# Performance work log

Measured on AMD Instinct MI355X. Metric: run time of the kernel, lower is better.

## Reference

```python
import jax, jax.numpy as jnp
import numpy as np

D_MODEL = 1024
N_EXPERTS = 16
TOP_K = 2
D_FF = 512      # per-expert SwiGLU hidden size
D_FF_SHARED = 1024
N_TOKENS = 4096


def setup_inputs() -> dict:
    key = jax.random.key(0)
    ks = jax.random.split(key, 9)
    s_in = 1.0 / np.sqrt(D_MODEL)
    s_ff = 1.0 / np.sqrt(D_FF)
    s_fs = 1.0 / np.sqrt(D_FF_SHARED)
    return {
        "hidden_states": jax.random.normal(ks[0], (N_TOKENS, D_MODEL), jnp.float32),
        "Wg": jax.random.normal(ks[1], (D_MODEL, N_EXPERTS), jnp.float32) * s_in,
        "w1": jax.random.normal(ks[2], (N_EXPERTS, D_MODEL, D_FF), jnp.float32) * s_in,
        "w3": jax.random.normal(ks[3], (N_EXPERTS, D_MODEL, D_FF), jnp.float32) * s_in,
        "w2": jax.random.normal(ks[4], (N_EXPERTS, D_FF, D_MODEL), jnp.float32) * s_ff,
        "ws1": jax.random.normal(ks[5], (D_MODEL, D_FF_SHARED), jnp.float32) * s_in,
        "ws3": jax.random.normal(ks[6], (D_MODEL, D_FF_SHARED), jnp.float32) * s_in,
        "ws2": jax.random.normal(ks[7], (D_FF_SHARED, D_MODEL), jnp.float32) * s_fs,
        "capacity": 1024,
    }


def reference(hidden_states, Wg, w1, w3, w2, ws1, ws3, ws2, capacity):
    T, d = hidden_states.shape
    E = Wg.shape[1]
    C = capacity

    # --- router: softmax in fp32, top-k, renormalize (norm_topk_prob=True) ---
    logits = hidden_states @ Wg                                  # [T, E]
    probs = jax.nn.softmax(logits.astype(jnp.float32), axis=-1)
    topw, topi = jax.lax.top_k(probs, TOP_K)                     # [T, K]
    topw = topw / jnp.sum(topw, axis=-1, keepdims=True)
    topw = topw.astype(hidden_states.dtype)

    # --- dispatch: flatten (token, k) pairs, compute slot within expert buffer ---
    flat_e = topi.reshape(-1)                                    # [T*K] expert id
    flat_t = jnp.repeat(jnp.arange(T), TOP_K)                    # [T*K] source token
    flat_w = topw.reshape(-1)                                    # [T*K]
    oh = jax.nn.one_hot(flat_e, E, dtype=jnp.int32)              # [T*K, E]
    # exclusive position of each pair within its expert's buffer
    pos = jnp.sum((jnp.cumsum(oh, axis=0) - 1) * oh, axis=-1)    # [T*K]
    keep = pos < C
    slot = jnp.where(keep, flat_e * C + pos, E * C)              # dropped -> dummy row

    buf = jnp.zeros((E * C + 1, d), hidden_states.dtype)
    buf = buf.at[slot].set(hidden_states[flat_t])
    xb = buf[: E * C].reshape(E, C, d)                           # [E, C, d]

    # --- per-expert SwiGLU MLP (grouped matmuls) ---
    h = jax.nn.silu(jnp.einsum("ecd,edf->ecf", xb, w1)) * jnp.einsum("ecd,edf->ecf", xb, w3)
    ob = jnp.einsum("ecf,efd->ecd", h, w2).reshape(E * C, d)     # [E*C, d]

    # --- weighted combine: gather expert outputs, scatter-add into token rows ---
    gathered = ob[jnp.minimum(slot, E * C - 1)]                  # [T*K, d]
    y = gathered * (flat_w * keep.astype(flat_w.dtype))[:, None]
    final = jnp.zeros_like(hidden_states).at[flat_t].add(y)

    # --- shared expert (dense SwiGLU over all tokens) ---
    sh = jax.nn.silu(hidden_states @ ws1) * (hidden_states @ ws3)
    final = final + sh @ ws2
    return final
```

## Files before the change

kernel.cpp:

```cpp
#include <hip/hip_runtime.h>
#include <stdint.h>

#define TT 4096
#define DM 1024
#define NE 16
#define DFF 512
#define DFS 1024
#define CAP 1024

typedef unsigned short u16;
typedef __bf16 bf16x8 __attribute__((ext_vector_type(8)));
typedef float f32x4 __attribute__((ext_vector_type(4)));

typedef __attribute__((address_space(1))) void as1_void;
typedef __attribute__((address_space(3))) void as3_void;

__device__ __forceinline__ u16 f2bf(float f) {
  union { float f; uint32_t u; } v; v.f = f;
  uint32_t u = v.u;
  u += 0x7fffu + ((u >> 16) & 1u);
  return (u16)(u >> 16);
}

__device__ __forceinline__ float bf2f(u16 b) {
  union { uint32_t u; float f; } v; v.u = ((uint32_t)b) << 16;
  return v.f;
}

__device__ __forceinline__ void gl2lds16(const void* g, void* l) {
  __builtin_amdgcn_global_load_lds(
      (as1_void*)(uintptr_t)g,
      (as3_void*)(uint32_t)(uintptr_t)l,
      16, 0, 0);
}

__global__ __launch_bounds__(256) void k_prep(
    const float* __restrict__ x, const float* __restrict__ Wg,
    const float* __restrict__ w1, const float* __restrict__ w3,
    const float* __restrict__ w2, const float* __restrict__ ws1,
    const float* __restrict__ ws3, const float* __restrict__ ws2,
    u16* __restrict__ hbf,
    u16* __restrict__ w1t, u16* __restrict__ w3t, u16* __restrict__ w2t,
    u16* __restrict__ ws1t, u16* __restrict__ ws3t, u16* __restrict__ ws2t,
    int* __restrict__ counts, int* __restrict__ tok_slot,
    int* __restrict__ tslot, float* __restrict__ tw) {
  __shared__ __align__(16) char smraw[18496];
  __shared__ int pick_e[32];
  __shared__ int base_sh[16];
  const int bid = blockIdx.x;
  const int tid = threadIdx.x;

  if (bid < 256) {
    float* x_lds = (float*)smraw;
    float (*lg)[17] = (float(*)[17])(smraw + 17408);
    const int e16 = tid & 15;
    const int kpc = tid >> 4;
    const int t0 = bid * 16;
    const int col = (tid & 63) * 4;
    const int rsub = tid >> 6;

    float acc[16];
#pragma unroll
    for (int t = 0; t < 16; ++t) acc[t] = 0.f;

    for (int q = 0; q < 4; ++q) {
      if (q) __syncthreads();
#pragma unroll
      for (int p = 0; p < 4; ++p) {
        int r = p * 4 + rsub;
        float4 xv = *(const float4*)&x[(size_t)(t0 + r) * DM + q * 256 + col];
        ushort4 o;
        o.x = f2bf(xv.x); o.y = f2bf(xv.y); o.z = f2bf(xv.z); o.w = f2bf(xv.w);
        *(ushort4*)&hbf[(size_t)(t0 + r) * DM + q * 256 + col] = o;
        *(float4*)&x_lds[r * 256 + col] = xv;
      }
      __syncthreads();
      float wg[16];
#pragma unroll
      for (int i = 0; i < 16; ++i)
        wg[i] = Wg[(size_t)(q * 256 + kpc * 16 + i) * NE + e16];
#pragma unroll
      for (int t = 0; t < 16; ++t) {
        const float4* xp = (const float4*)&x_lds[t * 256 + kpc * 16];
        float4 a0 = xp[0], a1 = xp[1], a2 = xp[2], a3 = xp[3];
        float s = acc[t];
        s += a0.x * wg[0]  + a0.y * wg[1]  + a0.z * wg[2]  + a0.w * wg[3];
        s += a1.x * wg[4]  + a1.y * wg[5]  + a1.z * wg[6]  + a1.w * wg[7];
        s += a2.x * wg[8]  + a2.y * wg[9]  + a2.z * wg[10] + a2.w * wg[11];
        s += a3.x * wg[12] + a3.y * wg[13] + a3.z * wg[14] + a3.w * wg[15];
        acc[t] = s;
      }
    }
    __syncthreads();
    float* red = (float*)smraw;
#pragma unroll
    for (int t = 0; t < 16; ++t) red[kpc * 272 + t * 16 + e16] = acc[t];
    __syncthreads();
    {
      int t2 = tid >> 4, e2 = tid & 15;
      float s = 0.f;
#pragma unroll
      for (int k2 = 0; k2 < 16; ++k2) s += red[k2 * 272 + t2 * 16 + e2];
      lg[t2][e2] = s;
    }
    __syncthreads();
    if (e16 == 0) {
      int tl = kpc;
      int t = t0 + tl;
      float b0 = -1e30f; int i0 = 0;
#pragma unroll
      for (int i = 0; i < NE; ++i) { float v = lg[tl][i]; if (v > b0) { b0 = v; i0 = i; } }
      float b1 = -1e30f; int i1 = 0;
#pragma unroll
      for (int i = 0; i < NE; ++i) { if (i == i0) continue; float v = lg[tl][i]; if (v > b1) { b1 = v; i1 = i; } }
      float ex = __expf(b1 - b0);
      float w0 = 1.f / (1.f + ex);
      float w1v = 1.f - w0;
      pick_e[2 * tl] = i0;
      pick_e[2 * tl + 1] = i1;
      tw[2 * t] = w0; tw[2 * t + 1] = w1v;
    }
    __syncthreads();
    if (tid < 16) {
      int c = 0;
#pragma unroll
      for (int j = 0; j < 32; ++j) c += (pick_e[j] == tid) ? 1 : 0;
      int base = 0;
      if (c > 0) base = atomicAdd(&counts[tid], c);
      base_sh[tid] = base;
    }
    __syncthreads();
    if (e16 == 0) {
      int tl = kpc;
      int t = t0 + tl;
#pragma unroll
      for (int kk = 0; kk < 2; ++kk) {
        int idx = 2 * tl + kk;
        int e = pick_e[idx];
        int rank = 0;
        for (int j = 0; j < idx; ++j) rank += (pick_e[j] == e) ? 1 : 0;
        int p = base_sh[e] + rank;
        int s = -1;
        if (p < CAP) { s = e * CAP + p; tok_slot[s] = t; }
        tslot[2 * t + kk] = s;
      }
    }
    return;
  }

  int tb = bid - 256;
  int z = tb >> 8, xy = tb & 255;
  const float* ip; u16* op; int R, C;
  if (z < 16)      { ip = w1 + (size_t)z * DM * DFF;       op = w1t + (size_t)z * DM * DFF;       R = DM;  C = DFF; }
  else if (z < 32) { int e = z - 16; ip = w3 + (size_t)e * DM * DFF; op = w3t + (size_t)e * DM * DFF; R = DM;  C = DFF; }
  else if (z < 48) { int e = z - 32; ip = w2 + (size_t)e * DFF * DM; op = w2t + (size_t)e * DFF * DM; R = DFF; C = DM; }
  else if (z == 48){ ip = ws1; op = ws1t; R = DM;  C = DFS; }
  else if (z == 49){ ip = ws3; op = ws3t; R = DM;  C = DFS; }
  else             { ip = ws2; op = ws2t; R = DFS; C = DM; }

  int c0 = (xy & 15) * 64, r0 = (xy >> 4) * 64;
  if (c0 >= C || r0 >= R) return;

  float (*tile)[65] = (float(*)[65])smraw;
  int tx = tid & 15, ty = tid >> 4;
#pragma unroll
  for (int j = 0; j < 4; ++j) {
    int r = ty + 16 * j;
    float4 v = *(const float4*)&ip[(size_t)(r0 + r) * C + c0 + tx * 4];
    *(float4*)&tile[r][tx * 4] = v;
  }
  __syncthreads();
#pragma unroll
  for (int j = 0; j < 4; ++j) {
    int c = ty + 16 * j;
    ushort4 o;
    o.x = f2bf(tile[tx * 4 + 0][c]);
    o.y = f2bf(tile[tx * 4 + 1][c]);
    o.z = f2bf(tile[tx * 4 + 2][c]);
    o.w = f2bf(tile[tx * 4 + 3][c]);
    *(ushort4*)&op[(size_t)(c0 + c) * R + r0 + tx * 4] = o;
  }
}

#define FRAG(BUF, ROW, CC)                                                       \
  (*(const bf16x8*)&BUF[(ROW) * 64 + ((((CC) * 4 + lq) ^ ((ROW) & 7)) << 3)])

__global__ __launch_bounds__(256) void k_up(
    const u16* __restrict__ hbf,
    const u16* __restrict__ ws1t, const u16* __restrict__ ws3t,
    const u16* __restrict__ w1t, const u16* __restrict__ w3t,
    u16* __restrict__ hs, u16* __restrict__ hexp,
    const int* __restrict__ counts, const int* __restrict__ tok_slot) {
  const int tid = threadIdx.x;
  const int nwg = 512 + NE * 64;
  int bid = (int)blockIdx.x;
  bid = (bid & 7) * (nwg >> 3) + (bid >> 3);

  const u16* B1p; const u16* B3p; u16* Cp;
  int m0, n0, N;
  int e = -1, cnt = 0;
  if (bid < 512) {
    m0 = (bid >> 4) * 128; n0 = (bid & 15) * 64;
    B1p = ws1t; B3p = ws3t; Cp = hs; N = DFS;
  } else {
    int r = bid - 512;
    e = r >> 6; int q = r & 63;
    m0 = (q >> 3) * 128; n0 = (q & 7) * 64;
    cnt = counts[e]; if (cnt > CAP) cnt = CAP;
    if (m0 >= cnt) return;
    B1p = w1t + (size_t)e * (DFF * DM);
    B3p = w3t + (size_t)e * (DFF * DM);
    Cp = hexp + (size_t)e * (CAP * DFF);
    N = DFF;
  }

  __shared__ __align__(16) u16 As[2][128 * 64];
  __shared__ __align__(16) u16 Bs1[2][64 * 64];
  __shared__ __align__(16) u16 Bs3[2][64 * 64];

  uint32_t aoff[4], boff[2];
#pragma unroll
  for (int j = 0; j < 4; ++j) {
    int L = tid + 256 * j;
    int row = L >> 3;
    int c = (L & 7) ^ (row & 7);
    int gr;
    if (e >= 0) {
      int rr = m0 + row;
      gr = (rr < cnt) ? tok_slot[e * CAP + rr] : 0;
    } else {
      gr = m0 + row;
    }
    aoff[j] = (uint32_t)gr * DM + c * 8;
  }
#pragma unroll
  for (int j = 0; j < 2; ++j) {
    int L = tid + 256 * j;
    int row = L >> 3;
    int c = (L & 7) ^ (row & 7);
    boff[j] = (uint32_t)(n0 + row) * DM + c * 8;
  }

  const int lane = tid & 63;
  const int wv = tid >> 6;
  const int wr = wv * 32;
  const int lr = lane & 15;
  const int lq = lane >> 4;

  f32x4 acc1[2][4], acc3[2][4];
#pragma unroll
  for (int i = 0; i < 2; ++i)
#pragma unroll
    for (int j = 0; j < 4; ++j) {
      acc1[i][j] = (f32x4){0.f, 0.f, 0.f, 0.f};
      acc3[i][j] = (f32x4){0.f, 0.f, 0.f, 0.f};
    }

#define UP_STAGE(B, K0)                                                              \
  do {                                                                               \
    _Pragma("unroll")                                                                \
    for (int j = 0; j < 4; ++j)                                                      \
      gl2lds16(hbf + aoff[j] + (K0), &As[B][(size_t)(tid + 256 * j) * 8]);           \
    _Pragma("unroll")                                                                \
    for (int j = 0; j < 2; ++j)                                                      \
      gl2lds16(B1p + boff[j] + (K0), &Bs1[B][(size_t)(tid + 256 * j) * 8]);          \
    _Pragma("unroll")                                                                \
    for (int j = 0; j < 2; ++j)                                                      \
      gl2lds16(B3p + boff[j] + (K0), &Bs3[B][(size_t)(tid + 256 * j) * 8]);          \
  } while (0)

#define UP_COMPUTE(B)                                                                \
  do {                                                                               \
    const u16* Ab = &As[B][0];                                                       \
    const u16* B1b = &Bs1[B][0];                                                     \
    const u16* B3b = &Bs3[B][0];                                                     \
    _Pragma("unroll")                                                                \
    for (int cc = 0; cc < 2; ++cc) {                                                 \
      bf16x8 af[2], bf1[4], bf3[4];                                                  \
      _Pragma("unroll")                                                              \
      for (int i = 0; i < 2; ++i) af[i] = FRAG(Ab, wr + i * 16 + lr, cc);            \
      _Pragma("unroll")                                                              \
      for (int j = 0; j < 4; ++j) {                                                  \
        bf1[j] = FRAG(B1b, j * 16 + lr, cc);                                         \
        bf3[j] = FRAG(B3b, j * 16 + lr, cc);                                         \
      }                                                                              \
      _Pragma("unroll")                                                              \
      for (int i = 0; i < 2; ++i)                                                    \
        _Pragma("unroll")                                                            \
        for (int j = 0; j < 4; ++j) {                                                \
          acc1[i][j] = __builtin_amdgcn_mfma_f32_16x16x32_bf16(af[i], bf1[j], acc1[i][j], 0, 0, 0); \
          acc3[i][j] = __builtin_amdgcn_mfma_f32_16x16x32_bf16(af[i], bf3[j], acc3[i][j], 0, 0, 0); \
        }                                                                            \
    }                                                                                \
  } while (0)

  UP_STAGE(0, 0);
  __syncthreads();
  int cur = 0;
  const int NT = DM / 64;
  for (int t = 0; t < NT - 1; ++t) {
    UP_STAGE(cur ^ 1, (t + 1) * 64);
    UP_COMPUTE(cur);
    __syncthreads();
    cur ^= 1;
  }
  UP_COMPUTE(cur);

#pragma unroll
  for (int i = 0; i < 2; ++i)
#pragma unroll
    for (int r = 0; r < 4; ++r) {
      int row = m0 + wr + i * 16 + lq * 4 + r;
      u16* crow = Cp + (size_t)row * N;
#pragma unroll
      for (int j = 0; j < 4; ++j) {
        float v1 = acc1[i][j][r];
        float v3 = acc3[i][j][r];
        float h = (v1 / (1.f + __expf(-v1))) * v3;
        crow[n0 + j * 16 + lr] = f2bf(h);
      }
    }
}

__global__ __launch_bounds__(256) void k_down(
    const u16* __restrict__ hs, const u16* __restrict__ ws2t,
    const u16* __restrict__ hexp, const u16* __restrict__ w2t,
    float* __restrict__ out, u16* __restrict__ ob,
    const int* __restrict__ counts) {
  const int tid = threadIdx.x;
  const int nwg = 512 + NE * 128;
  int bid = (int)blockIdx.x;
  bid = (bid & 7) * (nwg >> 3) + (bid >> 3);

  const u16* Ap; const u16* Bp;
  int m0, n0, K, e = -1;
  if (bid < 512) {
    m0 = (bid >> 4) * 128; n0 = (bid & 15) * 64;
    Ap = hs; Bp = ws2t; K = DFS;
  } else {
    int r = bid - 512;
    e = r >> 7; int q = r & 127;
    m0 = (q >> 4) * 128; n0 = (q & 15) * 64;
    int cnt = counts[e]; if (cnt > CAP) cnt = CAP;
    if (m0 >= cnt) return;
    Ap = hexp + (size_t)e * (CAP * DFF);
    Bp = w2t + (size_t)e * (DM * DFF);
    K = DFF;
  }

  __shared__ __align__(16) u16 As[2][128 * 64];
  __shared__ __align__(16) u16 Bs[2][64 * 64];

  uint32_t aoff[4], boff[2];
#pragma unroll
  for (int j = 0; j < 4; ++j) {
    int L = tid + 256 * j;
    int row = L >> 3;
    int c = (L & 7) ^ (row & 7);
    aoff[j] = (uint32_t)(m0 + row) * K + c * 8;
  }
#pragma unroll
  for (int j = 0; j < 2; ++j) {
    int L = tid + 256 * j;
    int row = L >> 3;
    int c = (L & 7) ^ (row & 7);
    boff[j] = (uint32_t)(n0 + row) * K + c * 8;
  }

  const int lane = tid & 63;
  const int wv = tid >> 6;
  const int wr = wv * 32;
  const int lr = lane & 15;
  const int lq = lane >> 4;

  f32x4 acc[2][4];
#pragma unroll
  for (int i = 0; i < 2; ++i)
#pragma unroll
    for (int j = 0; j < 4; ++j) acc[i][j] = (f32x4){0.f, 0.f, 0.f, 0.f};

#define DN_STAGE(B, K0)                                                              \
  do {                                                                               \
    _Pragma("unroll")                                                                \
    for (int j = 0; j < 4; ++j)                                                      \
      gl2lds16(Ap + aoff[j] + (K0), &As[B][(size_t)(tid + 256 * j) * 8]);            \
    _Pragma("unroll")                                                                \
    for (int j = 0; j < 2; ++j)                                                      \
      gl2lds16(Bp + boff[j] + (K0), &Bs[B][(size_t)(tid + 256 * j) * 8]);            \
  } while (0)

#define DN_COMPUTE(B)                                                                \
  do {                                                                               \
    const u16* Ab = &As[B][0];                                                       \
    const u16* Bb = &Bs[B][0];                                                       \
    _Pragma("unroll")                                                                \
    for (int cc = 0; cc < 2; ++cc) {                                                 \
      bf16x8 af[2], bfr[4];                                                          \
      _Pragma("unroll")                                                              \
      for (int i = 0; i < 2; ++i) af[i] = FRAG(Ab, wr + i * 16 + lr, cc);            \
      _Pragma("unroll")                                                              \
      for (int j = 0; j < 4; ++j) bfr[j] = FRAG(Bb, j * 16 + lr, cc);                \
      _Pragma("unroll")                                                              \
      for (int i = 0; i < 2; ++i)                                                    \
        _Pragma("unroll")                                                            \
        for (int j = 0; j < 4; ++j)                                                  \
          acc[i][j] = __builtin_amdgcn_mfma_f32_16x16x32_bf16(af[i], bfr[j], acc[i][j], 0, 0, 0); \
    }                                                                                \
  } while (0)

  DN_STAGE(0, 0);
  __syncthreads();
  int cur = 0;
  const int NT = K / 64;
  for (int t = 0; t < NT - 1; ++t) {
    DN_STAGE(cur ^ 1, (t + 1) * 64);
    DN_COMPUTE(cur);
    __syncthreads();
    cur ^= 1;
  }
  DN_COMPUTE(cur);

  if (e < 0) {
#pragma unroll
    for (int i = 0; i < 2; ++i)
#pragma unroll
      for (int r = 0; r < 4; ++r) {
        int row = m0 + wr + i * 16 + lq * 4 + r;
        float* orow = out + (size_t)row * DM;
#pragma unroll
        for (int j = 0; j < 4; ++j)
          orow[n0 + j * 16 + lr] = acc[i][j][r];
      }
  } else {
    u16* obase = ob + (size_t)e * CAP * DM;
#pragma unroll
    for (int i = 0; i < 2; ++i)
#pragma unroll
      for (int r = 0; r < 4; ++r) {
        int row = m0 + wr + i * 16 + lq * 4 + r;
        u16* orow = obase + (size_t)row * DM;
#pragma unroll
        for (int j = 0; j < 4; ++j)
          orow[n0 + j * 16 + lr] = f2bf(acc[i][j][r]);
      }
  }
}

__global__ __launch_bounds__(256) void k_combine(
    float* __restrict__ out, const u16* __restrict__ ob,
    const int* __restrict__ tslot, const float* __restrict__ tw) {
  int t = blockIdx.x;
  int c = threadIdx.x * 4;
  int s0 = tslot[2 * t], s1 = tslot[2 * t + 1];
  float w0 = tw[2 * t], w1 = tw[2 * t + 1];
  float4 v = *(float4*)&out[(size_t)t * DM + c];
  if (s0 >= 0) {
    ushort4 o = *(const ushort4*)&ob[(size_t)s0 * DM + c];
    v.x += w0 * bf2f(o.x); v.y += w0 * bf2f(o.y);
    v.z += w0 * bf2f(o.z); v.w += w0 * bf2f(o.w);
  }
  if (s1 >= 0) {
    ushort4 o = *(const ushort4*)&ob[(size_t)s1 * DM + c];
    v.x += w1 * bf2f(o.x); v.y += w1 * bf2f(o.y);
    v.z += w1 * bf2f(o.z); v.w += w1 * bf2f(o.w);
  }
  *(float4*)&out[(size_t)t * DM + c] = v;
}

extern "C" void kernel_launch(void* const* d_in, const int* in_sizes, int n_in,
                              void* d_out, int out_size, void* d_ws, size_t ws_size,
                              hipStream_t stream) {
  (void)in_sizes; (void)n_in; (void)out_size; (void)ws_size;
  const float* x   = (const float*)d_in[0];
  const float* Wg  = (const float*)d_in[1];
  const float* w1  = (const float*)d_in[2];
  const float* w3  = (const float*)d_in[3];
  const float* w2  = (const float*)d_in[4];
  const float* ws1 = (const float*)d_in[5];
  const float* ws3 = (const float*)d_in[6];
  const float* ws2 = (const float*)d_in[7];
  float* out = (float*)d_out;
  char* ws = (char*)d_ws;

  u16* hbf   = (u16*)(ws + 0);
  u16* w1t   = (u16*)(ws + 8388608);
  u16* w3t   = (u16*)(ws + 25165824);
  u16* w2t   = (u16*)(ws + 41943040);
  u16* ws1t  = (u16*)(ws + 58720256);
  u16* ws3t  = (u16*)(ws + 60817408);
  u16* ws2t  = (u16*)(ws + 62914560);
  u16* hs    = (u16*)(ws + 65011712);
  u16* hexp  = (u16*)(ws + 73400320);
  int* counts    = (int*)(ws + 90177536);
  int* tok_slot  = (int*)(ws + 90177792);
  int* tslot     = (int*)(ws + 90243328);
  float* tw      = (float*)(ws + 90276096);
  u16* ob    = (u16*)(ws + 0);

  hipMemsetAsync(counts, 0, NE * sizeof(int), stream);

  k_prep<<<dim3(256 + 51 * 256), dim3(256), 0, stream>>>(
      x, Wg, w1, w3, w2, ws1, ws3, ws2,
      hbf, w1t, w3t, w2t, ws1t, ws3t, ws2t,
      counts, tok_slot, tslot, tw);

  k_up<<<dim3(512 + NE * 64), dim3(256), 0, stream>>>(
      hbf, ws1t, ws3t, w1t, w3t, hs, hexp, counts, tok_slot);

  k_down<<<dim3(512 + NE * 128), dim3(256), 0, stream>>>(
      hs, ws2t, hexp, w2t, out, ob, counts);

  k_combine<<<dim3(TT), dim3(256), 0, stream>>>(out, ob, tslot, tw);
}
```

Before: 281.8 us.

## Retile up/down GEMMs to 128x128 output tiles with BK=32 and 2x2 waves

Changes both the up-projection and down-projection grouped GEMMs from 128x64 tiles with K-step 64 to 128x128 tiles with K-step 32. Work is split over a 2x2 wave grid, each wave holding a 64x64 accumulator block, and the LDS swizzle is adjusted for 32-wide rows. The larger tile raises arithmetic intensity per loaded byte and halves the number of workgroups. In exchange it doubles the per-wave accumulator registers (k_up holds 128 fp32 accumulators per lane), bounded by launch_bounds occupancy hints of 3 and 4, and adds more barriers per K.

```diff
diff --git a/kernel.cpp b/kernel.cpp
--- a/kernel.cpp
+++ b/kernel.cpp
@@ -182,30 +182,30 @@
   }
 }
 
-#define FRAG(BUF, ROW, CC)                                                       \
-  (*(const bf16x8*)&BUF[(ROW) * 64 + ((((CC) * 4 + lq) ^ ((ROW) & 7)) << 3)])
-
-__global__ __launch_bounds__(256) void k_up(
+#define FRAG32(BUF, ROW)                                                         \
+  (*(const bf16x8*)&BUF[(ROW) * 32 + (((lq) ^ (((ROW) >> 1) & 3)) << 3)])
+
+__global__ __launch_bounds__(256, 3) void k_up(
     const u16* __restrict__ hbf,
     const u16* __restrict__ ws1t, const u16* __restrict__ ws3t,
     const u16* __restrict__ w1t, const u16* __restrict__ w3t,
     u16* __restrict__ hs, u16* __restrict__ hexp,
     const int* __restrict__ counts, const int* __restrict__ tok_slot) {
   const int tid = threadIdx.x;
-  const int nwg = 512 + NE * 64;
+  const int nwg = 256 + NE * 32;
   int bid = (int)blockIdx.x;
   bid = (bid & 7) * (nwg >> 3) + (bid >> 3);
 
   const u16* B1p; const u16* B3p; u16* Cp;
   int m0, n0, N;
   int e = -1, cnt = 0;
-  if (bid < 512) {
-    m0 = (bid >> 4) * 128; n0 = (bid & 15) * 64;
+  if (bid < 256) {
+    m0 = (bid >> 3) * 128; n0 = (bid & 7) * 128;
     B1p = ws1t; B3p = ws3t; Cp = hs; N = DFS;
   } else {
-    int r = bid - 512;
-    e = r >> 6; int q = r & 63;
-    m0 = (q >> 3) * 128; n0 = (q & 7) * 64;
+    int r = bid - 256;
+    e = r >> 5; int q = r & 31;
+    m0 = (q >> 2) * 128; n0 = (q & 3) * 128;
     cnt = counts[e]; if (cnt > CAP) cnt = CAP;
     if (m0 >= cnt) return;
     B1p = w1t + (size_t)e * (DFF * DM);
@@ -214,16 +214,16 @@
     N = DFF;
   }
 
-  __shared__ __align__(16) u16 As[2][128 * 64];
-  __shared__ __align__(16) u16 Bs1[2][64 * 64];
-  __shared__ __align__(16) u16 Bs3[2][64 * 64];
-
-  uint32_t aoff[4], boff[2];
-#pragma unroll
-  for (int j = 0; j < 4; ++j) {
+  __shared__ __align__(16) u16 As[2][128 * 32];
+  __shared__ __align__(16) u16 Bs1[2][128 * 32];
+  __shared__ __align__(16) u16 Bs3[2][128 * 32];
+
+  uint32_t aoff[2], boff[2];
+#pragma unroll
+  for (int j = 0; j < 2; ++j) {
     int L = tid + 256 * j;
-    int row = L >> 3;
-    int c = (L & 7) ^ (row & 7);
+    int row = L >> 2;
+    int c = (L & 3) ^ ((row >> 1) & 3);
     int gr;
     if (e >= 0) {
       int rr = m0 + row;
@@ -236,20 +236,21 @@
 #pragma unroll
   for (int j = 0; j < 2; ++j) {
     int L = tid + 256 * j;
-    int row = L >> 3;
-    int c = (L & 7) ^ (row & 7);
+    int row = L >> 2;
+    int c = (L & 3) ^ ((row >> 1) & 3);
     boff[j] = (uint32_t)(n0 + row) * DM + c * 8;
   }
 
   const int lane = tid & 63;
   const int wv = tid >> 6;
-  const int wr = wv * 32;
+  const int wr = (wv >> 1) * 64;
+  const int wc = (wv & 1) * 64;
   const int lr = lane & 15;
   const int lq = lane >> 4;
 
-  f32x4 acc1[2][4], acc3[2][4];
-#pragma unroll
-  for (int i = 0; i < 2; ++i)
+  f32x4 acc1[4][4], acc3[4][4];
+#pragma unroll
+  for (int i = 0; i < 4; ++i)
 #pragma unroll
     for (int j = 0; j < 4; ++j) {
       acc1[i][j] = (f32x4){0.f, 0.f, 0.f, 0.f};
@@ -259,7 +260,7 @@
 #define UP_STAGE(B, K0)                                                              \
   do {                                                                               \
     _Pragma("unroll")                                                                \
-    for (int j = 0; j < 4; ++j)                                                      \
+    for (int j = 0; j < 2; ++j)                                                      \
       gl2lds16(hbf + aoff[j] + (K0), &As[B][(size_t)(tid + 256 * j) * 8]);           \
     _Pragma("unroll")                                                                \
     for (int j = 0; j < 2; ++j)                                                      \
@@ -274,32 +275,29 @@
     const u16* Ab = &As[B][0];                                                       \
     const u16* B1b = &Bs1[B][0];                                                     \
     const u16* B3b = &Bs3[B][0];                                                     \
-    _Pragma("unroll")                                                                \
-    for (int cc = 0; cc < 2; ++cc) {                                                 \
-      bf16x8 af[2], bf1[4], bf3[4];                                                  \
+    bf16x8 af[4];                                                                    \
+    _Pragma("unroll")                                                                \
+    for (int i = 0; i < 4; ++i) af[i] = FRAG32(Ab, wr + i * 16 + lr);                \
+    _Pragma("unroll")                                                                \
+    for (int j = 0; j < 4; ++j) {                                                    \
+      bf16x8 b1 = FRAG32(B1b, wc + j * 16 + lr);                                     \
       _Pragma("unroll")                                                              \
-      for (int i = 0; i < 2; ++i) af[i] = FRAG(Ab, wr + i * 16 + lr, cc);            \
+      for (int i = 0; i < 4; ++i)                                                    \
+        acc1[i][j] = __builtin_amdgcn_mfma_f32_16x16x32_bf16(af[i], b1, acc1[i][j], 0, 0, 0); \
+      bf16x8 b3 = FRAG32(B3b, wc + j * 16 + lr);                                     \
       _Pragma("unroll")                                                              \
-      for (int j = 0; j < 4; ++j) {                                                  \
-        bf1[j] = FRAG(B1b, j * 16 + lr, cc);                                         \
-        bf3[j] = FRAG(B3b, j * 16 + lr, cc);                                         \
-      }                                                                              \
-      _Pragma("unroll")                                                              \
-      for (int i = 0; i < 2; ++i)                                                    \
-        _Pragma("unroll")                                                            \
-        for (int j = 0; j < 4; ++j) {                                                \
-          acc1[i][j] = __builtin_amdgcn_mfma_f32_16x16x32_bf16(af[i], bf1[j], acc1[i][j], 0, 0, 0); \
-          acc3[i][j] = __builtin_amdgcn_mfma_f32_16x16x32_bf16(af[i], bf3[j], acc3[i][j], 0, 0, 0); \
-        }                                                                            \
+      for (int i = 0; i < 4; ++i)                                                    \
+        acc3[i][j] = __builtin_amdgcn_mfma_f32_16x16x32_bf16(af[i], b3, acc3[i][j], 0, 0, 0); \
     }                                                                                \
   } while (0)
 
   UP_STAGE(0, 0);
   __syncthreads();
   int cur = 0;
-  const int NT = DM / 64;
+  const int NT = DM / 32;
+#pragma unroll 1
   for (int t = 0; t < NT - 1; ++t) {
-    UP_STAGE(cur ^ 1, (t + 1) * 64);
+    UP_STAGE(cur ^ 1, (t + 1) * 32);
     UP_COMPUTE(cur);
     __syncthreads();
     cur ^= 1;
@@ -307,7 +305,7 @@
   UP_COMPUTE(cur);
 
 #pragma unroll
-  for (int i = 0; i < 2; ++i)
+  for (int i = 0; i < 4; ++i)
 #pragma unroll
     for (int r = 0; r < 4; ++r) {
       int row = m0 + wr + i * 16 + lq * 4 + r;
@@ -317,30 +315,30 @@
         float v1 = acc1[i][j][r];
         float v3 = acc3[i][j][r];
         float h = (v1 / (1.f + __expf(-v1))) * v3;
-        crow[n0 + j * 16 + lr] = f2bf(h);
+        crow[n0 + wc + j * 16 + lr] = f2bf(h);
       }
     }
 }
 
-__global__ __launch_bounds__(256) void k_down(
+__global__ __launch_bounds__(256, 4) void k_down(
     const u16* __restrict__ hs, const u16* __restrict__ ws2t,
     const u16* __restrict__ hexp, const u16* __restrict__ w2t,
     float* __restrict__ out, u16* __restrict__ ob,
     const int* __restrict__ counts) {
   const int tid = threadIdx.x;
-  const int nwg = 512 + NE * 128;
+  const int nwg = 256 + NE * 64;
   int bid = (int)blockIdx.x;
   bid = (bid & 7) * (nwg >> 3) + (bid >> 3);
 
   const u16* Ap; const u16* Bp;
   int m0, n0, K, e = -1;
-  if (bid < 512) {
-    m0 = (bid >> 4) * 128; n0 = (bid & 15) * 64;
+  if (bid < 256) {
+    m0 = (bid >> 3) * 128; n0 = (bid & 7) * 128;
     Ap = hs; Bp = ws2t; K = DFS;
   } else {
-    int r = bid - 512;
-    e = r >> 7; int q = r & 127;
-    m0 = (q >> 4) * 128; n0 = (q & 15) * 64;
+    int r = bid - 256;
+    e = r >> 6; int q = r & 63;
+    m0 = (q >> 3) * 128; n0 = (q & 7) * 128;
     int cnt = counts[e]; if (cnt > CAP) cnt = CAP;
     if (m0 >= cnt) return;
     Ap = hexp + (size_t)e * (CAP * DFF);
@@ -348,41 +346,36 @@
     K = DFF;
   }
 
-  __shared__ __align__(16) u16 As[2][128 * 64];
-  __shared__ __align__(16) u16 Bs[2][64 * 64];
-
-  uint32_t aoff[4], boff[2];
-#pragma unroll
-  for (int j = 0; j < 4; ++j) {
-    int L = tid + 256 * j;
-    int row = L >> 3;
-    int c = (L & 7) ^ (row & 7);
-    aoff[j] = (uint32_t)(m0 + row) * K + c * 8;
-  }
+  __shared__ __align__(16) u16 As[2][128 * 32];
+  __shared__ __align__(16) u16 Bs[2][128 * 32];
+
+  uint32_t aoff[2], boff[2];
 #pragma unroll
   for (int j = 0; j < 2; ++j) {
     int L = tid + 256 * j;
-    int row = L >> 3;
-    int c = (L & 7) ^ (row & 7);
+    int row = L >> 2;
+    int c = (L & 3) ^ ((row >> 1) & 3);
+    aoff[j] = (uint32_t)(m0 + row) * K + c * 8;
     boff[j] = (uint32_t)(n0 + row) * K + c * 8;
   }
 
   const int lane = tid & 63;
   const int wv = tid >> 6;
-  const int wr = wv * 32;
+  const int wr = (wv >> 1) * 64;
+  const int wc = (wv & 1) * 64;
   const int lr = lane & 15;
   const int lq = lane >> 4;
 
-  f32x4 acc[2][4];
-#pragma unroll
-  for (int i = 0; i < 2; ++i)
+  f32x4 acc[4][4];
+#pragma unroll
+  for (int i = 0; i < 4; ++i)
 #pragma unroll
     for (int j = 0; j < 4; ++j) acc[i][j] = (f32x4){0.f, 0.f, 0.f, 0.f};
 
 #define DN_STAGE(B, K0)                                                              \
   do {                                                                               \
     _Pragma("unroll")                                                                \
-    for (int j = 0; j < 4; ++j)                                                      \
+    for (int j = 0; j < 2; ++j)                                                      \
       gl2lds16(Ap + aoff[j] + (K0), &As[B][(size_t)(tid + 256 * j) * 8]);            \
     _Pragma("unroll")                                                                \
     for (int j = 0; j < 2; ++j)                                                      \
@@ -393,27 +386,25 @@
   do {                                                                               \
     const u16* Ab = &As[B][0];                                                       \
     const u16* Bb = &Bs[B][0];                                                       \
-    _Pragma("unroll")                                                                \
-    for (int cc = 0; cc < 2; ++cc) {                                                 \
-      bf16x8 af[2], bfr[4];                                                          \
+    bf16x8 af[4];                                                                    \
+    _Pragma("unroll")                                                                \
+    for (int i = 0; i < 4; ++i) af[i] = FRAG32(Ab, wr + i * 16 + lr);                \
+    _Pragma("unroll")                                                                \
+    for (int j = 0; j < 4; ++j) {                                                    \
+      bf16x8 br = FRAG32(Bb, wc + j * 16 + lr);                                      \
       _Pragma("unroll")                                                              \
-      for (int i = 0; i < 2; ++i) af[i] = FRAG(Ab, wr + i * 16 + lr, cc);            \
-      _Pragma("unroll")                                                              \
-      for (int j = 0; j < 4; ++j) bfr[j] = FRAG(Bb, j * 16 + lr, cc);                \
-      _Pragma("unroll")                                                              \
-      for (int i = 0; i < 2; ++i)                                                    \
-        _Pragma("unroll")                                                            \
-        for (int j = 0; j < 4; ++j)                                                  \
-          acc[i][j] = __builtin_amdgcn_mfma_f32_16x16x32_bf16(af[i], bfr[j], acc[i][j], 0, 0, 0); \
+      for (int i = 0; i < 4; ++i)                                                    \
+        acc[i][j] = __builtin_amdgcn_mfma_f32_16x16x32_bf16(af[i], br, acc[i][j], 0, 0, 0); \
     }                                                                                \
   } while (0)
 
   DN_STAGE(0, 0);
   __syncthreads();
   int cur = 0;
-  const int NT = K / 64;
+  const int NT = K / 32;
+#pragma unroll 1
   for (int t = 0; t < NT - 1; ++t) {
-    DN_STAGE(cur ^ 1, (t + 1) * 64);
+    DN_STAGE(cur ^ 1, (t + 1) * 32);
     DN_COMPUTE(cur);
     __syncthreads();
     cur ^= 1;
@@ -422,26 +413,26 @@
 
   if (e < 0) {
 #pragma unroll
-    for (int i = 0; i < 2; ++i)
+    for (int i = 0; i < 4; ++i)
 #pragma unroll
       for (int r = 0; r < 4; ++r) {
         int row = m0 + wr + i * 16 + lq * 4 + r;
         float* orow = out + (size_t)row * DM;
 #pragma unroll
         for (int j = 0; j < 4; ++j)
-          orow[n0 + j * 16 + lr] = acc[i][j][r];
+          orow[n0 + wc + j * 16 + lr] = acc[i][j][r];
       }
   } else {
     u16* obase = ob + (size_t)e * CAP * DM;
 #pragma unroll
-    for (int i = 0; i < 2; ++i)
+    for (int i = 0; i < 4; ++i)
 #pragma unroll
       for (int r = 0; r < 4; ++r) {
         int row = m0 + wr + i * 16 + lq * 4 + r;
         u16* orow = obase + (size_t)row * DM;
 #pragma unroll
         for (int j = 0; j < 4; ++j)
-          orow[n0 + j * 16 + lr] = f2bf(acc[i][j][r]);
+          orow[n0 + wc + j * 16 + lr] = f2bf(acc[i][j][r]);
       }
   }
 }
@@ -504,10 +495,10 @@
       hbf, w1t, w3t, w2t, ws1t, ws3t, ws2t,
       counts, tok_slot, tslot, tw);
 
-  k_up<<<dim3(512 + NE * 64), dim3(256), 0, stream>>>(
+  k_up<<<dim3(256 + NE * 32), dim3(256), 0, stream>>>(
       hbf, ws1t, ws3t, w1t, w3t, hs, hexp, counts, tok_slot);
 
-  k_down<<<dim3(512 + NE * 128), dim3(256), 0, stream>>>(
+  k_down<<<dim3(256 + NE * 64), dim3(256), 0, stream>>>(
       hs, ws2t, hexp, w2t, out, ob, counts);
 
   k_combine<<<dim3(TT), dim3(256), 0, stream>>>(out, ob, tslot, tw);
```

After: 279.5 us. Within noise of the previous version (-0.8%).
